# Performance work log

Hardware: AMD Instinct MI355X
Metric: run time of the kernel (lower is better)

The kernel has to match this reference:

```python
import jax, jax.numpy as jnp
import numpy as np


def _sin_rpe(Lq, d_model, dtype):
    # sinusoidal relative-position embeddings for positions -(Lq-1)..(Lq-1)
    inv_freq = 1.0 / (10000.0 ** (jnp.arange(0, d_model, 2, dtype=jnp.float32) / d_model))
    pos = jnp.arange(-(Lq - 1), Lq, dtype=jnp.float32)  # [2Lq-1]
    ang = pos[:, None] * inv_freq[None, :]               # [2Lq-1, d_model/2]
    emb = jnp.zeros((2 * Lq - 1, d_model), dtype=jnp.float32)
    emb = emb.at[:, 0::2].set(jnp.sin(ang)).at[:, 1::2].set(jnp.cos(ang))
    return emb.astype(dtype)


def _rel_shift(x):
    # Transformer-XL relative shift. x: [B,H,Lq,Lr] with Lr = 2Lq-1
    B, H, Lq, Lr = x.shape
    xp = jnp.concatenate([jnp.zeros((B, H, Lq, 1), x.dtype), x], axis=-1)
    xp = xp.reshape(B, H, Lr + 1, Lq)
    return xp[:, :, 1:].reshape(B, H, Lq, Lr)[..., Lr - Lq:]


def setup_inputs() -> dict:
    key = jax.random.key(0)
    ks = jax.random.split(key, 7)
    B, Lq, D, H = 1, 2048, 1024, 16
    d_head = D // H
    s = 0.02
    return {
        "w": jax.random.normal(ks[0], (B, Lq, D), jnp.float32),
        "Wq": jax.random.normal(ks[1], (D, D), jnp.float32) * s,
        "Wk": jax.random.normal(ks[2], (D, D), jnp.float32) * s,
        "Wv": jax.random.normal(ks[3], (D, D), jnp.float32) * s,
        "Wr": jax.random.normal(ks[4], (D, D), jnp.float32) * s,
        "u_bias": jax.random.normal(ks[5], (H, d_head), jnp.float32) * 0.02,
        "v_bias": jax.random.normal(ks[6], (H, d_head), jnp.float32) * 0.02,
    }


def reference(w, Wq, Wk, Wv, Wr, u_bias, v_bias):
    B, Lq, D = w.shape
    H, d_head = u_bias.shape
    scale = 1.0 / np.sqrt(d_head).astype(np.float32)
    r = _sin_rpe(Lq, D, w.dtype)                          # [2Lq-1, D]
    # torch Linear: y = x @ W.T
    q = (w @ Wq.T).reshape(B, Lq, H, d_head).transpose(0, 2, 1, 3)  # [B,H,Lq,d]
    k = (w @ Wk.T).reshape(B, Lq, H, d_head).transpose(0, 2, 1, 3)
    v = (w @ Wv.T).reshape(B, Lq, H, d_head).transpose(0, 2, 1, 3)
    rp = (r @ Wr.T).reshape(2 * Lq - 1, H, d_head).transpose(1, 0, 2)  # [H,2Lq-1,d]
    AC = jnp.einsum('bhid,bhjd->bhij', q + u_bias[None, :, None, :], k)   # [B,H,Lq,Lq]
    BD = jnp.einsum('bhid,hjd->bhij', q + v_bias[None, :, None, :], rp)   # [B,H,Lq,2Lq-1]
    BD = _rel_shift(BD)                                                   # [B,H,Lq,Lq]
    attn = jax.nn.softmax((AC + BD) * scale, axis=-1)
    out = jnp.einsum('bhij,bhjd->bhid', attn, v)          # [B,H,Lq,d]
    return out.transpose(0, 2, 1, 3).reshape(B, Lq, D)
```

## Files before the change

### kernel.cpp

```cpp
#include <hip/hip_runtime.h>
#include <math.h>
#include <stddef.h>

#define LQ 2048
#define DM 1024
#define NH 16
#define DH 64
#define LR 4095

typedef __attribute__((ext_vector_type(4))) float f4v;
typedef __attribute__((ext_vector_type(8))) short s8v;
typedef __attribute__((ext_vector_type(2))) unsigned short us2;
typedef __attribute__((ext_vector_type(8))) unsigned short us8;
typedef __attribute__((ext_vector_type(2))) unsigned int u32x2;
typedef __attribute__((ext_vector_type(4))) unsigned int u32x4;

__device__ __forceinline__ unsigned short f2bf(float x) {
    unsigned int u = __float_as_uint(x);
    return (unsigned short)((u + 0x7FFFu + ((u >> 16) & 1u)) >> 16);
}
__device__ __forceinline__ float bf2f(unsigned short s) {
    return __uint_as_float(((unsigned int)s) << 16);
}
__device__ __forceinline__ unsigned cvtpk(float lo, float hi) {
    unsigned r;
    asm("v_cvt_pk_bf16_f32 %0, %1, %2" : "=v"(r) : "v"(lo), "v"(hi));
    return r;
}
template<int CTRL>
__device__ __forceinline__ float rot16(float x) {
    return __uint_as_float((unsigned)__builtin_amdgcn_update_dpp(
        0, (int)__float_as_uint(x), CTRL, 0xF, 0xF, false));
}
#define GLOAD16(g, l) __builtin_amdgcn_global_load_lds((g), (l), 16, 0, 0)
#define WAVE_LDS_FENCE() do { \
    asm volatile("s_waitcnt lgkmcnt(0)" ::: "memory"); \
    __builtin_amdgcn_sched_barrier(0); } while (0)

#define MFMA16(a, b, c) __builtin_amdgcn_mfma_f32_16x16x32_bf16((a), (b), (c), 0, 0, 0)

__device__ __forceinline__ s8v sw_read8(const unsigned short* base, int row, int colshort) {
    int byte = (row * 128 + colshort * 2) ^ ((row & 7) << 4);
    return *(const s8v*)((const char*)base + byte);
}

__global__ __launch_bounds__(256)
void prep(const float* __restrict__ w, const float* __restrict__ Wq,
          const float* __restrict__ Wk, const float* __restrict__ Wv,
          const float* __restrict__ Wr, unsigned short* __restrict__ dst,
          unsigned short* __restrict__ r, unsigned short* __restrict__ rpg) {
    int b = blockIdx.x;
    if (b < 3072) {
        size_t e0 = ((size_t)b * 256 + threadIdx.x) * 8;
        const float* src;
        if (e0 < (size_t)LQ * DM) src = w + e0;
        else {
            size_t ro = e0 - (size_t)LQ * DM;
            int wi = (int)(ro >> 20);
            size_t off = ro & 1048575;
            src = (wi == 0 ? Wq : wi == 1 ? Wk : wi == 2 ? Wv : Wr) + off;
        }
        f4v a = *(const f4v*)src;
        f4v c = *(const f4v*)(src + 4);
        us8 o;
        o[0]=f2bf(a[0]); o[1]=f2bf(a[1]); o[2]=f2bf(a[2]); o[3]=f2bf(a[3]);
        o[4]=f2bf(c[0]); o[5]=f2bf(c[1]); o[6]=f2bf(c[2]); o[7]=f2bf(c[3]);
        *(us8*)(dst + e0) = o;
    } else if (b < 11262) {
        int tg = (b - 3072) * 256 + threadIdx.x;
        int gm = tg >> 9, c2 = tg & 511;
        float invf = expf(-(float)c2 * (9.210340371976184f / 512.0f));
        float ang = (float)(gm - (LQ - 1)) * invf;
        us2 o; o[0] = f2bf(sinf(ang)); o[1] = f2bf(cosf(ang));
        *(us2*)&r[(size_t)gm * DM + c2 * 2] = o;
    } else {
        int idx = (b - 11262) * 2048 + threadIdx.x * 8;
        unsigned short* p = (idx < 131072)
            ? (rpg - 131072 + idx)
            : (rpg + (size_t)LR * DM + (idx - 131072));
        *(us8*)p = (us8){0,0,0,0,0,0,0,0};
    }
}

__global__ __launch_bounds__(256)
void proj_all(const unsigned short* __restrict__ wbf, const unsigned short* __restrict__ rr,
              const unsigned short* __restrict__ Wqb, const unsigned short* __restrict__ Wkb,
              const unsigned short* __restrict__ Wvb, const unsigned short* __restrict__ Wrb,
              unsigned short* __restrict__ qb, unsigned short* __restrict__ kkb,
              unsigned short* __restrict__ vtg, unsigned short* __restrict__ rpg) {
    __shared__ unsigned short As[64 * 64];
    __shared__ unsigned short Bs[128 * 64];
    int bid = blockIdx.x;
    int mat, mblk, nblk;
    if (bid < 768) { mat = bid >> 8; int rm = bid & 255; mblk = rm >> 3; nblk = rm & 7; }
    else           { mat = 3; int rm = bid - 768; mblk = rm >> 3; nblk = rm & 7; }
    const int M = (mat < 3) ? LQ : LR;
    const unsigned short* A = (mat < 3) ? wbf : rr;
    const unsigned short* B = mat == 0 ? Wqb : mat == 1 ? Wkb : mat == 2 ? Wvb : Wrb;
    unsigned short* C = mat == 0 ? qb : mat == 1 ? kkb : mat == 2 ? vtg : rpg;
    const int m0 = mblk * 64, n0 = nblk * 128;
    const int t = threadIdx.x;
    const int w = t >> 6, lan16 = t & 15, lgrp = (t & 63) >> 4;
    const int wm = (w >> 1) * 32, wn = (w & 1) * 64;
    f4v acc[2][4] = {};

    for (int k0 = 0; k0 < DM; k0 += 64) {
        #pragma unroll
        for (int it = 0; it < 2; ++it) {
            int slot = it * 256 + t;
            int row = slot >> 3, c8 = slot & 7;
            int gm = m0 + row; if (gm > M - 1) gm = M - 1;
            GLOAD16(A + (size_t)gm * DM + k0 + c8 * 8,
                    (char*)As + (size_t)(it * 256 + w * 64) * 16);
        }
        #pragma unroll
        for (int it = 0; it < 4; ++it) {
            int slot = it * 256 + t;
            int row = slot >> 3, c8 = slot & 7;
            GLOAD16(B + (size_t)(n0 + row) * DM + k0 + c8 * 8,
                    (char*)Bs + (size_t)(it * 256 + w * 64) * 16);
        }
        __syncthreads();
        #pragma unroll
        for (int kk = 0; kk < 2; ++kk) {
            s8v aF[2], bF[4];
            #pragma unroll
            for (int i = 0; i < 2; ++i)
                aF[i] = *(const s8v*)&As[(wm + i * 16 + lan16) * 64 + kk * 32 + lgrp * 8];
            #pragma unroll
            for (int j = 0; j < 4; ++j)
                bF[j] = *(const s8v*)&Bs[(wn + j * 16 + lan16) * 64 + kk * 32 + lgrp * 8];
            #pragma unroll
            for (int i = 0; i < 2; ++i)
                #pragma unroll
                for (int j = 0; j < 4; ++j)
                    acc[i][j] = MFMA16(aF[i], bF[j], acc[i][j]);
        }
        __syncthreads();
    }
    if (mat != 2) {
        #pragma unroll
        for (int i = 0; i < 2; ++i)
            #pragma unroll
            for (int j = 0; j < 4; ++j)
                #pragma unroll
                for (int rg = 0; rg < 4; ++rg) {
                    int row = m0 + wm + i * 16 + lgrp * 4 + rg;
                    if (row < M)
                        C[(size_t)row * DM + n0 + wn + j * 16 + lan16] = f2bf(acc[i][j][rg]);
                }
    } else {
        #pragma unroll
        for (int i = 0; i < 2; ++i)
            #pragma unroll
            for (int j = 0; j < 4; ++j) {
                int n = n0 + wn + j * 16 + lan16;
                int m = m0 + wm + i * 16 + lgrp * 4;
                u32x2 pp;
                pp[0] = cvtpk(acc[i][j][0], acc[i][j][1]);
                pp[1] = cvtpk(acc[i][j][2], acc[i][j][3]);
                *(u32x2*)&C[(size_t)n * LQ + m] = pp;
            }
    }
}

__global__ __launch_bounds__(256, 2)
void attn_mfma(const unsigned short* __restrict__ q, const unsigned short* __restrict__ kkg,
               const unsigned short* __restrict__ vtg, const unsigned short* __restrict__ rpg,
               const float* __restrict__ ub, const float* __restrict__ vb,
               float* __restrict__ Oa, float* __restrict__ Ob,
               float* __restrict__ la, float* __restrict__ lb) {
    __shared__ unsigned short Kb[2][64 * 64];
    __shared__ unsigned short Bb[2][128 * 64];
    __shared__ unsigned short Vb[64 * 64];
    __shared__ unsigned short Gtw[4][80 * 20];
    __shared__ unsigned short Pt[4][64 * 18];

    const int dd = blockIdx.x;
    const int f = (dd & 7) * 128 + (dd >> 3);
    const int h = f >> 6;
    const int sp = (f >> 5) & 1;
    const int i0 = (f & 31) * 64;
    const int col0 = h * DH;
    float* Op = sp ? Ob : Oa;
    float* lp = sp ? lb : la;
    const int jbeg = sp * 1024;

    const int t = threadIdx.x;
    const int w = t >> 6, lan16 = t & 15, lgrp = (t & 63) >> 4;
    const int W = w * 16;
    const int cbase = 48 - W;
    const float C1 = 0.125f * 1.4426950408889634f;
    const float C0 = -4.0f * 1.4426950408889634f;

    unsigned short* gw = Gtw[w];
    unsigned short* pw = Pt[w];

    union uv { u32x4 u; s8v s; };
    auto mkfrag = [&](int gi, const float* bias, s8v* dstf) {
        #pragma unroll
        for (int kk = 0; kk < 2; ++kk) {
            int cb = kk * 32 + lgrp * 8;
            us8 qv = (us8){0,0,0,0,0,0,0,0};
            if (gi < LQ) qv = *(const us8*)(q + (size_t)gi * DM + col0 + cb);
            f4v b0 = *(const f4v*)(bias + col0 + cb);
            f4v b1 = *(const f4v*)(bias + col0 + cb + 4);
            uv o;
            o.u[0] = cvtpk(bf2f(qv[0]) + b0[0], bf2f(qv[1]) + b0[1]);
            o.u[1] = cvtpk(bf2f(qv[2]) + b0[2], bf2f(qv[3]) + b0[3]);
            o.u[2] = cvtpk(bf2f(qv[4]) + b1[0], bf2f(qv[5]) + b1[1]);
            o.u[3] = cvtpk(bf2f(qv[6]) + b1[2], bf2f(qv[7]) + b1[3]);
            dstf[kk] = o.s;
        }
    };
    s8v quF[2], qvlF[2], qvsF[2];
    mkfrag(i0 + W + lan16, ub, quF);
    mkfrag(i0 + W + lan16, vb, qvlF);
    mkfrag(i0 + W + 1 + lan16, vb, qvsF);

    auto stageK = [&](int j0, int buf) {
        #pragma unroll
        for (int it = 0; it < 2; ++it) {
            int slot = it * 256 + t;
            int row = slot >> 3, c8 = (t & 7) ^ (row & 7);
            GLOAD16(kkg + (size_t)(j0 + row) * DM + col0 + c8 * 8,
                    (char*)&Kb[buf][0] + (size_t)(it * 256 + (t & ~63)) * 16);
        }
    };
    auto stageB = [&](int rel, int buf) {
        int base = (rel <= 0) ? rel + 4031 : rel - 65;
        #pragma unroll
        for (int it = 0; it < 4; ++it) {
            int slot = it * 256 + t;
            int row = slot >> 3, c8 = (t & 7) ^ (row & 7);
            GLOAD16(rpg + (ptrdiff_t)(base + row) * DM + col0 + c8 * 8,
                    (char*)&Bb[buf][0] + (size_t)(it * 256 + (t & ~63)) * 16);
        }
    };
    auto stageV = [&](int j0) {
        #pragma unroll
        for (int it = 0; it < 2; ++it) {
            int slot = it * 256 + t;
            int row = slot >> 3, c8 = (t & 7) ^ (row & 7);
            GLOAD16(vtg + (size_t)(col0 + row) * LQ + j0 + c8 * 8,
                    (char*)&Vb[0] + (size_t)(it * 256 + (t & ~63)) * 16);
        }
    };

    f4v accO[4] = {};
    float lsum[4] = {0.f, 0.f, 0.f, 0.f};

    stageK(jbeg, 0);
    stageB(jbeg - i0, 0);

    int cur = 0;
    for (int tt = 0; tt < 16; ++tt) {
        const int j0 = jbeg + tt * 64;
        const int rel = j0 - i0;
        stageV(j0);
        const int tn = (tt < 15) ? tt + 1 : 15;
        stageK(jbeg + tn * 64, cur ^ 1);
        stageB(jbeg + tn * 64 - i0, cur ^ 1);
        __builtin_amdgcn_sched_barrier(0);
        asm volatile("s_waitcnt vmcnt(8)" ::: "memory");
        __builtin_amdgcn_s_barrier();
        __builtin_amdgcn_sched_barrier(0);

        f4v acF[4] = {};
        #pragma unroll
        for (int nf = 0; nf < 4; ++nf)
            #pragma unroll
            for (int kk = 0; kk < 2; ++kk) {
                s8v bF = sw_read8(&Kb[cur][0], nf * 16 + lan16, kk * 32 + lgrp * 8);
                acF[nf] = MFMA16(quF[kk], bF, acF[nf]);
            }
        f4v g[5] = {};
        {
            const s8v* qf = (rel <= 0) ? qvlF : qvsF;
            #pragma unroll
            for (int c = 0; c < 5; ++c)
                #pragma unroll
                for (int kk = 0; kk < 2; ++kk) {
                    s8v bF = sw_read8(&Bb[cur][0], cbase + c * 16 + lan16, kk * 32 + lgrp * 8);
                    g[c] = MFMA16(qf[kk], bF, g[c]);
                }
        }
        if (rel == 0) {
            #pragma unroll
            for (int c = 0; c < 5; ++c) {
                int trow = -65 + cbase + c * 16 + lan16;
                const unsigned short* bp = rpg + (ptrdiff_t)trow * DM + col0;
                #pragma unroll
                for (int kk = 0; kk < 2; ++kk) {
                    us8 bv = *(const us8*)(bp + kk * 32 + lgrp * 8);
                    g[c] = MFMA16(qvsF[kk], (s8v)bv, g[c]);
                }
            }
        }
        #pragma unroll
        for (int c = 0; c < 5; ++c) {
            int cl = c * 16 + lan16;
            u32x2 pp;
            pp[0] = cvtpk(g[c][0], g[c][1]);
            pp[1] = cvtpk(g[c][2], g[c][3]);
            *(u32x2*)&gw[cl * 20 + lgrp * 4] = pp;
        }
        WAVE_LDS_FENCE();

        #pragma unroll
        for (int nf = 0; nf < 4; ++nf) {
            int jl = nf * 16 + lan16;
            float pp[4];
            #pragma unroll
            for (int rg = 0; rg < 4; ++rg) {
                const int rhat = lgrp * 4 + rg;
                float bd = bf2f(gw[(jl - rhat + 15) * 20 + rhat]);
                pp[rg] = exp2f(fmaf(acF[nf][rg] + bd, C1, C0));
                lsum[rg] += pp[rg];
            }
            *(unsigned*)&pw[jl * 18 + lgrp * 4]     = cvtpk(pp[0], pp[1]);
            *(unsigned*)&pw[jl * 18 + lgrp * 4 + 2] = cvtpk(pp[2], pp[3]);
        }
        WAVE_LDS_FENCE();

        s8v pF[2];
        #pragma unroll
        for (int kk = 0; kk < 2; ++kk) {
            us8 tmp;
            #pragma unroll
            for (int e = 0; e < 8; ++e)
                tmp[e] = pw[(kk * 32 + lgrp * 8 + e) * 18 + lan16];
            pF[kk] = (s8v)tmp;
        }
        __builtin_amdgcn_sched_barrier(0);
        asm volatile("s_waitcnt vmcnt(6)" ::: "memory");
        __builtin_amdgcn_s_barrier();
        __builtin_amdgcn_sched_barrier(0);

        #pragma unroll
        for (int nf = 0; nf < 4; ++nf)
            #pragma unroll
            for (int kk = 0; kk < 2; ++kk) {
                s8v vF = sw_read8(&Vb[0], nf * 16 + lan16, kk * 32 + lgrp * 8);
                accO[nf] = MFMA16(pF[kk], vF, accO[nf]);
            }
        __builtin_amdgcn_sched_barrier(0);
        __builtin_amdgcn_s_barrier();
        __builtin_amdgcn_sched_barrier(0);
        cur ^= 1;
    }

    #pragma unroll
    for (int rg = 0; rg < 4; ++rg) {
        float s = lsum[rg];
        s += rot16<0x121>(s);
        s += rot16<0x122>(s);
        s += rot16<0x124>(s);
        s += rot16<0x128>(s);
        const int row = i0 + W + lgrp * 4 + rg;
        if (lan16 == 0) lp[h * LQ + row] = s;
        #pragma unroll
        for (int nf = 0; nf < 4; ++nf)
            Op[(size_t)row * DM + col0 + nf * 16 + lan16] = accO[nf][rg];
    }
}

__global__ __launch_bounds__(256)
void combine(const float* __restrict__ Oa, const float* __restrict__ Ob,
             const float* __restrict__ la, const float* __restrict__ lb,
             float* __restrict__ out) {
    int i = blockIdx.x * 256 + threadIdx.x;
    int e0 = i * 4;
    int row = e0 >> 10;
    int h = (e0 & 1023) >> 6;
    float inv = 1.f / (la[h * LQ + row] + lb[h * LQ + row]);
    f4v a = *(const f4v*)(Oa + e0);
    f4v b = *(const f4v*)(Ob + e0);
    f4v o = (a + b) * inv;
    *(f4v*)(out + e0) = o;
}

extern "C" void kernel_launch(void* const* d_in, const int* in_sizes, int n_in,
                              void* d_out, int out_size, void* d_ws, size_t ws_size,
                              hipStream_t stream) {
    const float* w  = (const float*)d_in[0];
    const float* Wq = (const float*)d_in[1];
    const float* Wk = (const float*)d_in[2];
    const float* Wv = (const float*)d_in[3];
    const float* Wr = (const float*)d_in[4];
    const float* ub = (const float*)d_in[5];
    const float* vb = (const float*)d_in[6];
    float* out = (float*)d_out;

    const size_t U = 1048576;
    unsigned short* ws = (unsigned short*)d_ws;
    unsigned short* wbf = ws;
    unsigned short* Wqb = ws + 2 * U;
    unsigned short* Wkb = ws + 3 * U;
    unsigned short* Wvb = ws + 4 * U;
    unsigned short* Wrb = ws + 5 * U;
    unsigned short* qb  = ws + 6 * U;
    unsigned short* kkb = ws + 8 * U;
    unsigned short* vtg = ws + 10 * U;
    unsigned short* rpg = ws + 12 * U + 131072;
    unsigned short* r   = rpg + (size_t)LR * DM + 131072;

    float* Oa = (float*)r;
    float* Ob = (float*)ws;
    float* la = (float*)(ws + 4 * U);
    float* lb = la + NH * LQ;

    dim3 blk(256);
    hipLaunchKernelGGL(prep, dim3(11390), blk, 0, stream, w, Wq, Wk, Wv, Wr, wbf, r, rpg);
    hipLaunchKernelGGL(proj_all, dim3(1280), blk, 0, stream,
                       wbf, r, Wqb, Wkb, Wvb, Wrb, qb, kkb, vtg, rpg);
    hipLaunchKernelGGL(attn_mfma, dim3(1024), blk, 0, stream,
                       qb, kkb, vtg, rpg, ub, vb, Oa, Ob, la, lb);
    hipLaunchKernelGGL(combine, dim3(2048), blk, 0, stream, Oa, Ob, la, lb, out);
}
```

Measured before the change: 141.3 us.

## Enlarge projection tiles and restructure attention to load V directly into registers

The projection GEMM moves from 64x128 to 128x128 tiles, halving the grid and reusing each loaded B tile across twice as many rows. The attention kernel drops the V LDS buffer and the separate P buffer and single-buffers K. V fragments are loaded straight from global memory into registers, and P reuses the per-wave G scratch. The smaller LDS footprint allows raising launch bounds to 3 blocks per SM, and s_setprio hints are added around the MFMA sections. Risks include more register pressure from the V registers and the larger accumulators, less latency hiding once K is single-buffered, and uncoalesced per-lane V loads.

```diff
diff --git a/kernel.cpp b/kernel.cpp
--- a/kernel.cpp
+++ b/kernel.cpp
@@ -88,50 +88,44 @@
               const unsigned short* __restrict__ Wvb, const unsigned short* __restrict__ Wrb,
               unsigned short* __restrict__ qb, unsigned short* __restrict__ kkb,
               unsigned short* __restrict__ vtg, unsigned short* __restrict__ rpg) {
-    __shared__ unsigned short As[64 * 64];
+    __shared__ unsigned short As[128 * 64];
     __shared__ unsigned short Bs[128 * 64];
     int bid = blockIdx.x;
     int mat, mblk, nblk;
-    if (bid < 768) { mat = bid >> 8; int rm = bid & 255; mblk = rm >> 3; nblk = rm & 7; }
-    else           { mat = 3; int rm = bid - 768; mblk = rm >> 3; nblk = rm & 7; }
+    if (bid < 384) { mat = bid >> 7; int rm = bid & 127; mblk = rm >> 3; nblk = rm & 7; }
+    else           { mat = 3; int rm = bid - 384; mblk = rm >> 3; nblk = rm & 7; }
     const int M = (mat < 3) ? LQ : LR;
     const unsigned short* A = (mat < 3) ? wbf : rr;
     const unsigned short* B = mat == 0 ? Wqb : mat == 1 ? Wkb : mat == 2 ? Wvb : Wrb;
     unsigned short* C = mat == 0 ? qb : mat == 1 ? kkb : mat == 2 ? vtg : rpg;
-    const int m0 = mblk * 64, n0 = nblk * 128;
+    const int m0 = mblk * 128, n0 = nblk * 128;
     const int t = threadIdx.x;
     const int w = t >> 6, lan16 = t & 15, lgrp = (t & 63) >> 4;
-    const int wm = (w >> 1) * 32, wn = (w & 1) * 64;
-    f4v acc[2][4] = {};
+    const int wm = (w >> 1) * 64, wn = (w & 1) * 64;
+    f4v acc[4][4] = {};
 
     for (int k0 = 0; k0 < DM; k0 += 64) {
         #pragma unroll
-        for (int it = 0; it < 2; ++it) {
+        for (int it = 0; it < 4; ++it) {
             int slot = it * 256 + t;
             int row = slot >> 3, c8 = slot & 7;
             int gm = m0 + row; if (gm > M - 1) gm = M - 1;
             GLOAD16(A + (size_t)gm * DM + k0 + c8 * 8,
-                    (char*)As + (size_t)(it * 256 + w * 64) * 16);
-        }
-        #pragma unroll
-        for (int it = 0; it < 4; ++it) {
-            int slot = it * 256 + t;
-            int row = slot >> 3, c8 = slot & 7;
+                    (char*)As + (size_t)(it * 256 + (t & ~63)) * 16);
             GLOAD16(B + (size_t)(n0 + row) * DM + k0 + c8 * 8,
-                    (char*)Bs + (size_t)(it * 256 + w * 64) * 16);
+                    (char*)Bs + (size_t)(it * 256 + (t & ~63)) * 16);
         }
         __syncthreads();
         #pragma unroll
         for (int kk = 0; kk < 2; ++kk) {
-            s8v aF[2], bF[4];
-            #pragma unroll
-            for (int i = 0; i < 2; ++i)
+            s8v aF[4], bF[4];
+            #pragma unroll
+            for (int i = 0; i < 4; ++i) {
                 aF[i] = *(const s8v*)&As[(wm + i * 16 + lan16) * 64 + kk * 32 + lgrp * 8];
-            #pragma unroll
-            for (int j = 0; j < 4; ++j)
-                bF[j] = *(const s8v*)&Bs[(wn + j * 16 + lan16) * 64 + kk * 32 + lgrp * 8];
-            #pragma unroll
-            for (int i = 0; i < 2; ++i)
+                bF[i] = *(const s8v*)&Bs[(wn + i * 16 + lan16) * 64 + kk * 32 + lgrp * 8];
+            }
+            #pragma unroll
+            for (int i = 0; i < 4; ++i)
                 #pragma unroll
                 for (int j = 0; j < 4; ++j)
                     acc[i][j] = MFMA16(aF[i], bF[j], acc[i][j]);
@@ -140,7 +134,7 @@
     }
     if (mat != 2) {
         #pragma unroll
-        for (int i = 0; i < 2; ++i)
+        for (int i = 0; i < 4; ++i)
             #pragma unroll
             for (int j = 0; j < 4; ++j)
                 #pragma unroll
@@ -151,7 +145,7 @@
                 }
     } else {
         #pragma unroll
-        for (int i = 0; i < 2; ++i)
+        for (int i = 0; i < 4; ++i)
             #pragma unroll
             for (int j = 0; j < 4; ++j) {
                 int n = n0 + wn + j * 16 + lan16;
@@ -164,17 +158,15 @@
     }
 }
 
-__global__ __launch_bounds__(256, 2)
+__global__ __launch_bounds__(256, 3)
 void attn_mfma(const unsigned short* __restrict__ q, const unsigned short* __restrict__ kkg,
                const unsigned short* __restrict__ vtg, const unsigned short* __restrict__ rpg,
                const float* __restrict__ ub, const float* __restrict__ vb,
                float* __restrict__ Oa, float* __restrict__ Ob,
                float* __restrict__ la, float* __restrict__ lb) {
-    __shared__ unsigned short Kb[2][64 * 64];
+    __shared__ unsigned short Kb[64 * 64];
     __shared__ unsigned short Bb[2][128 * 64];
-    __shared__ unsigned short Vb[64 * 64];
-    __shared__ unsigned short Gtw[4][80 * 20];
-    __shared__ unsigned short Pt[4][64 * 18];
+    __shared__ unsigned short Gtw[4][1600];
 
     const int dd = blockIdx.x;
     const int f = (dd & 7) * 128 + (dd >> 3);
@@ -194,7 +186,6 @@
     const float C0 = -4.0f * 1.4426950408889634f;
 
     unsigned short* gw = Gtw[w];
-    unsigned short* pw = Pt[w];
 
     union uv { u32x4 u; s8v s; };
     auto mkfrag = [&](int gi, const float* bias, s8v* dstf) {
@@ -217,14 +208,15 @@
     mkfrag(i0 + W + lan16, ub, quF);
     mkfrag(i0 + W + lan16, vb, qvlF);
     mkfrag(i0 + W + 1 + lan16, vb, qvsF);
-
-    auto stageK = [&](int j0, int buf) {
+    __builtin_amdgcn_sched_barrier(0);
+
+    auto stageK = [&](int j0) {
         #pragma unroll
         for (int it = 0; it < 2; ++it) {
             int slot = it * 256 + t;
             int row = slot >> 3, c8 = (t & 7) ^ (row & 7);
             GLOAD16(kkg + (size_t)(j0 + row) * DM + col0 + c8 * 8,
-                    (char*)&Kb[buf][0] + (size_t)(it * 256 + (t & ~63)) * 16);
+                    (char*)&Kb[0] + (size_t)(it * 256 + (t & ~63)) * 16);
         }
     };
     auto stageB = [&](int rel, int buf) {
@@ -237,41 +229,40 @@
                     (char*)&Bb[buf][0] + (size_t)(it * 256 + (t & ~63)) * 16);
         }
     };
-    auto stageV = [&](int j0) {
-        #pragma unroll
-        for (int it = 0; it < 2; ++it) {
-            int slot = it * 256 + t;
-            int row = slot >> 3, c8 = (t & 7) ^ (row & 7);
-            GLOAD16(vtg + (size_t)(col0 + row) * LQ + j0 + c8 * 8,
-                    (char*)&Vb[0] + (size_t)(it * 256 + (t & ~63)) * 16);
-        }
-    };
 
     f4v accO[4] = {};
     float lsum[4] = {0.f, 0.f, 0.f, 0.f};
 
-    stageK(jbeg, 0);
+    stageK(jbeg);
     stageB(jbeg - i0, 0);
 
     int cur = 0;
     for (int tt = 0; tt < 16; ++tt) {
         const int j0 = jbeg + tt * 64;
         const int rel = j0 - i0;
-        stageV(j0);
-        const int tn = (tt < 15) ? tt + 1 : 15;
-        stageK(jbeg + tn * 64, cur ^ 1);
-        stageB(jbeg + tn * 64 - i0, cur ^ 1);
+
+        us8 vreg[4][2];
+        #pragma unroll
+        for (int nf = 0; nf < 4; ++nf)
+            #pragma unroll
+            for (int kk = 0; kk < 2; ++kk) {
+                const unsigned short* vp =
+                    vtg + (size_t)(col0 + nf * 16 + lan16) * LQ + j0 + kk * 32 + lgrp * 8;
+                asm volatile("global_load_dwordx4 %0, %1, off"
+                             : "=&v"(vreg[nf][kk]) : "v"(vp));
+            }
         __builtin_amdgcn_sched_barrier(0);
         asm volatile("s_waitcnt vmcnt(8)" ::: "memory");
         __builtin_amdgcn_s_barrier();
         __builtin_amdgcn_sched_barrier(0);
 
+        __builtin_amdgcn_s_setprio(1);
         f4v acF[4] = {};
         #pragma unroll
         for (int nf = 0; nf < 4; ++nf)
             #pragma unroll
             for (int kk = 0; kk < 2; ++kk) {
-                s8v bF = sw_read8(&Kb[cur][0], nf * 16 + lan16, kk * 32 + lgrp * 8);
+                s8v bF = sw_read8(&Kb[0], nf * 16 + lan16, kk * 32 + lgrp * 8);
                 acF[nf] = MFMA16(quF[kk], bF, acF[nf]);
             }
         f4v g[5] = {};
@@ -285,6 +276,7 @@
                     g[c] = MFMA16(qf[kk], bF, g[c]);
                 }
         }
+        __builtin_amdgcn_s_setprio(0);
         if (rel == 0) {
             #pragma unroll
             for (int c = 0; c < 5; ++c) {
@@ -297,6 +289,13 @@
                 }
             }
         }
+        __builtin_amdgcn_sched_barrier(0);
+        __builtin_amdgcn_s_barrier();
+        __builtin_amdgcn_sched_barrier(0);
+        const int tn = (tt < 15) ? tt + 1 : 15;
+        stageK(jbeg + tn * 64);
+        stageB(jbeg + tn * 64 - i0, cur ^ 1);
+
         #pragma unroll
         for (int c = 0; c < 5; ++c) {
             int cl = c * 16 + lan16;
@@ -307,19 +306,27 @@
         }
         WAVE_LDS_FENCE();
 
+        float gval[16];
+        #pragma unroll
+        for (int nf = 0; nf < 4; ++nf)
+            #pragma unroll
+            for (int rg = 0; rg < 4; ++rg) {
+                const int rhat = lgrp * 4 + rg;
+                gval[nf * 4 + rg] = bf2f(gw[(nf * 16 + lan16 - rhat + 15) * 20 + rhat]);
+            }
+        WAVE_LDS_FENCE();
+
         #pragma unroll
         for (int nf = 0; nf < 4; ++nf) {
             int jl = nf * 16 + lan16;
             float pp[4];
             #pragma unroll
             for (int rg = 0; rg < 4; ++rg) {
-                const int rhat = lgrp * 4 + rg;
-                float bd = bf2f(gw[(jl - rhat + 15) * 20 + rhat]);
-                pp[rg] = exp2f(fmaf(acF[nf][rg] + bd, C1, C0));
+                pp[rg] = exp2f(fmaf(acF[nf][rg] + gval[nf * 4 + rg], C1, C0));
                 lsum[rg] += pp[rg];
             }
-            *(unsigned*)&pw[jl * 18 + lgrp * 4]     = cvtpk(pp[0], pp[1]);
-            *(unsigned*)&pw[jl * 18 + lgrp * 4 + 2] = cvtpk(pp[2], pp[3]);
+            *(unsigned*)&gw[jl * 20 + lgrp * 4]     = cvtpk(pp[0], pp[1]);
+            *(unsigned*)&gw[jl * 20 + lgrp * 4 + 2] = cvtpk(pp[2], pp[3]);
         }
         WAVE_LDS_FENCE();
 
@@ -329,24 +336,20 @@
             us8 tmp;
             #pragma unroll
             for (int e = 0; e < 8; ++e)
-                tmp[e] = pw[(kk * 32 + lgrp * 8 + e) * 18 + lan16];
+                tmp[e] = gw[(kk * 32 + lgrp * 8 + e) * 20 + lan16];
             pF[kk] = (s8v)tmp;
         }
         __builtin_amdgcn_sched_barrier(0);
         asm volatile("s_waitcnt vmcnt(6)" ::: "memory");
-        __builtin_amdgcn_s_barrier();
-        __builtin_amdgcn_sched_barrier(0);
-
+        __builtin_amdgcn_sched_barrier(0);
+
+        __builtin_amdgcn_s_setprio(1);
         #pragma unroll
         for (int nf = 0; nf < 4; ++nf)
             #pragma unroll
-            for (int kk = 0; kk < 2; ++kk) {
-                s8v vF = sw_read8(&Vb[0], nf * 16 + lan16, kk * 32 + lgrp * 8);
-                accO[nf] = MFMA16(pF[kk], vF, accO[nf]);
-            }
-        __builtin_amdgcn_sched_barrier(0);
-        __builtin_amdgcn_s_barrier();
-        __builtin_amdgcn_sched_barrier(0);
+            for (int kk = 0; kk < 2; ++kk)
+                accO[nf] = MFMA16(pF[kk], (s8v)vreg[nf][kk], accO[nf]);
+        __builtin_amdgcn_s_setprio(0);
         cur ^= 1;
     }
 
@@ -412,7 +415,7 @@
 
     dim3 blk(256);
     hipLaunchKernelGGL(prep, dim3(11390), blk, 0, stream, w, Wq, Wk, Wv, Wr, wbf, r, rpg);
-    hipLaunchKernelGGL(proj_all, dim3(1280), blk, 0, stream,
+    hipLaunchKernelGGL(proj_all, dim3(640), blk, 0, stream,
                        wbf, r, Wqb, Wkb, Wvb, Wrb, qb, kkb, vtg, rpg);
     hipLaunchKernelGGL(attn_mfma, dim3(1024), blk, 0, stream,
                        qb, kkb, vtg, rpg, ub, vb, Oa, Ob, la, lb);
```

Result: slower. 293.9 us (+107.9%).
